# Optimization experiments

Hardware: AMD Instinct MI355X
Metric: run time of the kernel (lower is better)

## Reference

```python
import jax, jax.numpy as jnp
import numpy as np

NX, NY = 512, 1024  # scaled grid (source used 128x256)
HID = 32


def _grid_edges(nx, ny):
    """Bidirectional 4-neighbor grid adjacency as [2, E] int32."""
    idx = np.arange(nx * ny).reshape(nx, ny)
    h_s, h_t = idx[:, :-1].ravel(), idx[:, 1:].ravel()
    v_s, v_t = idx[:-1, :].ravel(), idx[1:, :].ravel()
    src = np.concatenate([h_s, h_t, v_s, v_t])
    dst = np.concatenate([h_t, h_s, v_t, v_s])
    return jnp.asarray(np.stack([src, dst]), dtype=jnp.int32)


def setup_inputs() -> dict:
    key = jax.random.key(0)
    ks = jax.random.split(key, 8)

    def lin(k, fan_in, fan_out):
        bound = 1.0 / np.sqrt(fan_in)
        kw, kb = jax.random.split(k)
        w = jax.random.uniform(kw, (fan_in, fan_out), jnp.float32, -bound, bound)
        b = jax.random.uniform(kb, (fan_out,), jnp.float32, -bound, bound)
        return w, b

    inp = {}
    inp["x"] = jax.random.normal(ks[0], (NX * NY, 4), jnp.float32)
    inp["edge_index_0"] = _grid_edges(NX, NY)
    inp["edge_index_1"] = _grid_edges(NX // 2, NY // 2)
    inp["edge_index_2"] = _grid_edges(NX // 4, NY // 4)
    inp["fc1_w"], inp["fc1_b"] = lin(ks[1], 4, HID)
    for i in range(1, 6):
        inp[f"w{i}"], inp[f"b{i}"] = lin(ks[1 + i], HID, HID)
    inp["fc2_w"], inp["fc2_b"] = lin(ks[7], HID, 2)
    return inp


def gcn_conv(x, edge_index, w, b):
    """PyG GCNConv: self-loops + symmetric norm + linear + scatter-add + bias."""
    n = x.shape[0]
    loop = jnp.arange(n, dtype=edge_index.dtype)
    src = jnp.concatenate([edge_index[0], loop])
    dst = jnp.concatenate([edge_index[1], loop])
    deg = jax.ops.segment_sum(jnp.ones(dst.shape, x.dtype), dst, num_segments=n)
    dis = jax.lax.rsqrt(deg)  # deg >= 1 because of self-loops
    norm = dis[src] * dis[dst]  # [E+N]
    xw = x @ w  # [N, HID]
    out = jax.ops.segment_sum(xw[src] * norm[:, None], dst, num_segments=n)
    return out + b


def _upsample2(x):
    # Buffer-exact replica of torch `upsample(x, dim=2, channels=32, scale=2)`:
    # with `channels` doubling between iterations; then transpose + reshape.
    x = x.T  # [32, N]
    ch = HID
    for _ in range(2):
        x = jnp.repeat(x.reshape(ch, -1), 2, axis=-1)
        ch *= 2
    return x.T.reshape(-1, HID)  # [4N, 32]


def reference(x, edge_index_0, edge_index_1, edge_index_2,
              fc1_w, fc1_b, w1, b1, w2, b2, w3, b3, w4, b4, w5, b5,
              fc2_w, fc2_b):
    nx1, ny1 = NX // 2, NY // 2
    h = jax.nn.relu(x @ fc1_w + fc1_b)
    h = jax.nn.relu(gcn_conv(h, edge_index_0, w1, b1))            # level 0
    h1 = h.reshape(NX, NY, HID)[::2, ::2, :].reshape(-1, HID)     # down to level 1
    h1 = jax.nn.relu(gcn_conv(h1, edge_index_1, w2, b2))
    h2 = h1.reshape(nx1, ny1, HID)[::2, ::2, :].reshape(-1, HID)  # down to level 2
    h2 = jax.nn.relu(gcn_conv(h2, edge_index_2, w3, b3))
    h1u = h1 + _upsample2(h2)                                     # up to level 1
    h1u = jax.nn.relu(gcn_conv(h1u, edge_index_1, w4, b4))
    hu = h + _upsample2(h1u)                                      # up to level 0
    hu = jax.nn.relu(gcn_conv(hu, edge_index_0, w5, b5))
    return hu @ fc2_w + fc2_b  # [NX*NY, 2]
```

## Files before the change

### kernel.cpp

```cpp
#include <hip/hip_runtime.h>


#define TI 4
#define TJ 32

typedef float v2f __attribute__((ext_vector_type(2)));

__device__ __forceinline__ v2f pka(v2f a, v2f b) {
  v2f d; asm("v_pk_add_f32 %0, %1, %2" : "=v"(d) : "v"(a), "v"(b)); return d;
}
__device__ __forceinline__ v2f pkm(v2f a, v2f b) {
  v2f d; asm("v_pk_mul_f32 %0, %1, %2" : "=v"(d) : "v"(a), "v"(b)); return d;
}
__device__ __forceinline__ v2f relu2(v2f a) {
  v2f d; d.x = fmaxf(a.x, 0.f); d.y = fmaxf(a.y, 0.f); return d;
}
__device__ __forceinline__ v2f pkfma_bl(v2f a, v2f b, v2f c) {
  v2f d;
  asm("v_pk_fma_f32 %0, %1, %2, %3 op_sel:[0,0,0] op_sel_hi:[0,1,1]"
      : "=v"(d) : "v"(a), "v"(b), "v"(c));
  return d;
}
__device__ __forceinline__ v2f pkfma_bh(v2f a, v2f b, v2f c) {
  v2f d;
  asm("v_pk_fma_f32 %0, %1, %2, %3 op_sel:[1,0,0] op_sel_hi:[1,1,1]"
      : "=v"(d) : "v"(a), "v"(b), "v"(c));
  return d;
}

__device__ __forceinline__ v2f LOq(const float4& f) { return *(const v2f*)&f.x; }
__device__ __forceinline__ v2f HIq(const float4& f) { return *(const v2f*)&f.z; }
__device__ __forceinline__ float4 MK4(v2f lo, v2f hi) {
  return make_float4(lo.x, lo.y, hi.x, hi.y);
}
__device__ __forceinline__ float4 p4add(float4 a, float4 b) {
  return MK4(pka(LOq(a), LOq(b)), pka(HIq(a), HIq(b)));
}

__device__ __forceinline__ float disf(int i, int j, int nx, int ny) {
  int deg = 1 + (i > 0) + (i < nx - 1) + (j > 0) + (j < ny - 1);
  return rsqrtf((float)deg);
}
__device__ __forceinline__ float4 f4z() { return make_float4(0.f, 0.f, 0.f, 0.f); }

template <int MODE, int NX, int NY, int NLOW>
__device__ __forceinline__ float4 load_u(
    const float* __restrict__ src, const float* __restrict__ low,
    const float4 (&f1c)[4], const float4& f1b, int gi, int gj, int c) {
  if (gi < 0 || gi >= NX || gj < 0 || gj >= NY) return f4z();
  const float d = disf(gi, gj, NX, NY);
  if constexpr (MODE == 0) {
    const float4 xv = ((const float4*)src)[gi * NY + gj];
    const v2f x01 = LOq(xv), x23 = HIq(xv);
    v2f h01 = LOq(f1b), h23 = HIq(f1b);
    h01 = pkfma_bl(x01, LOq(f1c[0]), h01); h23 = pkfma_bl(x01, HIq(f1c[0]), h23);
    h01 = pkfma_bh(x01, LOq(f1c[1]), h01); h23 = pkfma_bh(x01, HIq(f1c[1]), h23);
    h01 = pkfma_bl(x23, LOq(f1c[2]), h01); h23 = pkfma_bl(x23, HIq(f1c[2]), h23);
    h01 = pkfma_bh(x23, LOq(f1c[3]), h01); h23 = pkfma_bh(x23, HIq(f1c[3]), h23);
    h01 = relu2(h01); h23 = relu2(h23);
    v2f dp; dp.x = d; dp.y = d;
    return MK4(pkm(dp, h01), pkm(dp, h23));
  } else if constexpr (MODE == 1) {
    const float4 v = ((const float4*)src)[((size_t)(2 * gi) * (2 * NY) + 2 * gj) * 8 + c];
    v2f dp; dp.x = d; dp.y = d;
    return MK4(pkm(dp, LOq(v)), pkm(dp, HIq(v)));
  } else {
    const int r = gi * NY + gj;
    float4 v = ((const float4*)src)[(size_t)r * 8 + c];
    const int col = 16 * (r & 1) + 2 * c;
    const float2 E = *(const float2*)(low + (size_t)(r >> 3) * 32 + col);
    const float2 O = *(const float2*)(low + (size_t)((NLOW + (r >> 2)) >> 1) * 32 + col);
    v.x = (v.x + E.x) * d; v.y = (v.y + O.x) * d;
    v.z = (v.z + E.y) * d; v.w = (v.w + O.y) * d;
    return v;
  }
}

template <int MODE, int NX, int NY, int NLOW>
__global__ __launch_bounds__(256, 6) void fused_gcn(
    const float* __restrict__ src, const float* __restrict__ low,
    const float* __restrict__ w, const float* __restrict__ bias,
    const float* __restrict__ fc1w, const float* __restrict__ fc1b,
    const float* __restrict__ fw2, const float* __restrict__ fb2,
    float* __restrict__ out) {
  __shared__ __align__(16) float sT[32][TI * TJ + 2];
  __shared__ __align__(16) float ldsW[1024];
  __shared__ __align__(16) float ldsB[104];

  const int t = threadIdx.x;
  ((float4*)ldsW)[t] = ((const float4*)w)[t];
  if (t < 32) ldsB[t] = bias[t];
  if constexpr (MODE == 3) {
    if (t >= 32 && t < 96) ldsB[t] = fw2[t - 32];
    if (t >= 96 && t < 98) ldsB[t] = fb2[t - 96];
  }

  constexpr int GX = NY / TJ;
  constexpr int GY = NX / TI;
  constexpr int NWG = GX * GY;
  constexpr int LGX = (GX == 8) ? 3 : ((GX == 16) ? 4 : 5);
  const int bid = blockIdx.y * GX + blockIdx.x;
  const int sw = (bid & 7) * (NWG >> 3) + (bid >> 3);
  const int j0 = (sw & (GX - 1)) * TJ;
  const int i0 = (sw >> LGX) * TI;

  const int jn = t >> 3, c = t & 7;
  const int gj = j0 + jn;

  float4 f1c[4], f1b;
  if constexpr (MODE == 0) {
#pragma unroll
    for (int r = 0; r < 4; ++r) f1c[r] = *(const float4*)(fc1w + r * 32 + 4 * c);
    f1b = *(const float4*)(fc1b + 4 * c);
  }
  auto LOADU = [&](int a, int b) -> float4 {
    return load_u<MODE, NX, NY, NLOW>(src, low, f1c, f1b, a, b, c);
  };

  float4 up = LOADU(i0 - 1, gj);
  float4 uc = LOADU(i0, gj);
  float4 un = LOADU(i0 + 1, gj);
  float4 lf = LOADU(i0, gj - 1);
  float4 rt = LOADU(i0, gj + 1);

#pragma unroll
  for (int i = 0; i < TI; ++i) {
    const float4 sv = p4add(p4add(p4add(up, uc), p4add(un, lf)), rt);
    const int n = i * TJ + jn;
    sT[4 * c + 0][n] = sv.x; sT[4 * c + 1][n] = sv.y;
    sT[4 * c + 2][n] = sv.z; sT[4 * c + 3][n] = sv.w;
    if (i < TI - 1) {
      up = uc; uc = un;
      un = LOADU(i0 + i + 2, gj);
      lf = LOADU(i0 + i + 1, gj - 1);
      rt = LOADU(i0 + i + 1, gj + 1);
    }
  }
  __syncthreads();

  const int p = t >> 2, tc = t & 3;
  v2f oA[4] = {{0.f, 0.f}, {0.f, 0.f}, {0.f, 0.f}, {0.f, 0.f}};
  v2f oB[4] = {{0.f, 0.f}, {0.f, 0.f}, {0.f, 0.f}, {0.f, 0.f}};
#pragma unroll
  for (int k = 0; k < 32; ++k) {
    const v2f sp = *(const v2f*)&sT[k][2 * p];
    const float4 w0 = *(const float4*)&ldsW[k * 32 + 8 * tc];
    const float4 w1 = *(const float4*)&ldsW[k * 32 + 8 * tc + 4];
    const v2f w00 = LOq(w0), w01 = HIq(w0), w10 = LOq(w1), w11 = HIq(w1);
    oA[0] = pkfma_bl(sp, w00, oA[0]); oA[1] = pkfma_bl(sp, w01, oA[1]);
    oA[2] = pkfma_bl(sp, w10, oA[2]); oA[3] = pkfma_bl(sp, w11, oA[3]);
    oB[0] = pkfma_bh(sp, w00, oB[0]); oB[1] = pkfma_bh(sp, w01, oB[1]);
    oB[2] = pkfma_bh(sp, w10, oB[2]); oB[3] = pkfma_bh(sp, w11, oB[3]);
  }

  const int nA = 2 * p;
  const int gi = i0 + (nA >> 5);
  const int gjA = j0 + (nA & 31);
  const float dA = disf(gi, gjA, NX, NY);
  const float dB = disf(gi, gjA + 1, NX, NY);
  v2f dAp; dAp.x = dA; dAp.y = dA;
  v2f dBp; dBp.x = dB; dBp.y = dB;

  v2f bp[4];
  bp[0] = *(const v2f*)&ldsB[8 * tc];     bp[1] = *(const v2f*)&ldsB[8 * tc + 2];
  bp[2] = *(const v2f*)&ldsB[8 * tc + 4]; bp[3] = *(const v2f*)&ldsB[8 * tc + 6];

  v2f vA[4], vB[4];
#pragma unroll
  for (int q = 0; q < 4; ++q) {
    vA[q] = relu2(pkfma_bl(dAp, oA[q], bp[q]));
    vB[q] = relu2(pkfma_bl(dBp, oB[q], bp[q]));
  }

  if constexpr (MODE != 3) {
    float* opA = out + (size_t)(gi * NY + gjA) * 32 + 8 * tc;
    *(float4*)opA = MK4(vA[0], vA[1]);
    *(float4*)(opA + 4) = MK4(vA[2], vA[3]);
    *(float4*)(opA + 32) = MK4(vB[0], vB[1]);
    *(float4*)(opA + 36) = MK4(vB[2], vB[3]);
  } else {
    v2f accA = {0.f, 0.f}, accB = {0.f, 0.f};
#pragma unroll
    for (int q = 0; q < 4; ++q) {
      const v2f f0 = *(const v2f*)&ldsB[32 + 16 * tc + 4 * q];
      const v2f f1 = *(const v2f*)&ldsB[32 + 16 * tc + 4 * q + 2];
      accA = pkfma_bl(vA[q], f0, accA); accA = pkfma_bh(vA[q], f1, accA);
      accB = pkfma_bl(vB[q], f0, accB); accB = pkfma_bh(vB[q], f1, accB);
    }
#pragma unroll
    for (int m = 1; m <= 2; m <<= 1) {
      accA.x += __shfl_xor(accA.x, m, 64); accA.y += __shfl_xor(accA.y, m, 64);
      accB.x += __shfl_xor(accB.x, m, 64); accB.y += __shfl_xor(accB.y, m, 64);
    }
    if (tc == 0) {
      const v2f fb = *(const v2f*)&ldsB[96];
      accA = pka(accA, fb); accB = pka(accB, fb);
      ((float4*)out)[(gi * NY + gjA) >> 1] = MK4(accA, accB);
    }
  }
}

#define N0 (512 * 1024)
#define N1 (256 * 512)
#define N2 (128 * 256)

extern "C" void kernel_launch(void* const* d_in, const int* in_sizes, int n_in,
                              void* d_out, int out_size, void* d_ws, size_t ws_size,
                              hipStream_t stream) {
  const float* x    = (const float*)d_in[0];
  const float* fc1w = (const float*)d_in[4];
  const float* fc1b = (const float*)d_in[5];
  const float* w1 = (const float*)d_in[6];
  const float* b1 = (const float*)d_in[7];
  const float* w2 = (const float*)d_in[8];
  const float* b2 = (const float*)d_in[9];
  const float* w3 = (const float*)d_in[10];
  const float* b3 = (const float*)d_in[11];
  const float* w4 = (const float*)d_in[12];
  const float* b4 = (const float*)d_in[13];
  const float* w5 = (const float*)d_in[14];
  const float* b5 = (const float*)d_in[15];
  const float* fw2 = (const float*)d_in[16];
  const float* fb2 = (const float*)d_in[17];

  float* ws = (float*)d_ws;
  const size_t S0 = (size_t)N0 * 32, S1 = (size_t)N1 * 32, S2 = (size_t)N2 * 32;
  float* h   = ws;
  float* h1  = ws + S0;
  float* h2  = ws + S0 + S1;
  float* h1u = ws + S0 + S1 + S2;
  float* outp = (float*)d_out;

  fused_gcn<0, 512, 1024, 0><<<dim3(1024 / TJ, 512 / TI), 256, 0, stream>>>(
      x, nullptr, w1, b1, fc1w, fc1b, nullptr, nullptr, h);
  fused_gcn<1, 256, 512, 0><<<dim3(512 / TJ, 256 / TI), 256, 0, stream>>>(
      h, nullptr, w2, b2, nullptr, nullptr, nullptr, nullptr, h1);
  fused_gcn<1, 128, 256, 0><<<dim3(256 / TJ, 128 / TI), 256, 0, stream>>>(
      h1, nullptr, w3, b3, nullptr, nullptr, nullptr, nullptr, h2);
  fused_gcn<2, 256, 512, N2><<<dim3(512 / TJ, 256 / TI), 256, 0, stream>>>(
      h1, h2, w4, b4, nullptr, nullptr, nullptr, nullptr, h1u);
  fused_gcn<3, 512, 1024, N1><<<dim3(1024 / TJ, 512 / TI), 256, 0, stream>>>(
      h, h1u, w5, b5, nullptr, nullptr, fw2, fb2, outp);
}
```

Measured before the change: 198.9 us.

## Double row tile and compute four nodes per thread in GCN matmul

Raises the tile height from 4 to 8 rows so each thread computes 4 nodes × 8 outputs, loading a float4 of aggregated features per k-step instead of a float2. The goal is more FMAs per LDS weight load and more rows of vertical stencil reuse per tile, with fewer halo reloads. The shared-memory channel layout is permuted and its stride padded to limit bank conflicts. In exchange it uses more registers and LDS per block, so launch bounds drop from 6 to 4 waves per SIMD, which lowers occupancy.

```diff
diff --git a/kernel.cpp b/kernel.cpp
--- a/kernel.cpp
+++ b/kernel.cpp
@@ -1,8 +1,9 @@
 #include <hip/hip_runtime.h>
 
 
-#define TI 4
+#define TI 8
 #define TJ 32
+#define SSTR (TI * TJ + 4)
 
 typedef float v2f __attribute__((ext_vector_type(2)));
 
@@ -77,13 +78,13 @@
 }
 
 template <int MODE, int NX, int NY, int NLOW>
-__global__ __launch_bounds__(256, 6) void fused_gcn(
+__global__ __launch_bounds__(256, 4) void fused_gcn(
     const float* __restrict__ src, const float* __restrict__ low,
     const float* __restrict__ w, const float* __restrict__ bias,
     const float* __restrict__ fc1w, const float* __restrict__ fc1b,
     const float* __restrict__ fw2, const float* __restrict__ fb2,
     float* __restrict__ out) {
-  __shared__ __align__(16) float sT[32][TI * TJ + 2];
+  __shared__ __align__(16) float sT[32][SSTR];
   __shared__ __align__(16) float ldsW[1024];
   __shared__ __align__(16) float ldsB[104];
 
@@ -127,8 +128,10 @@
   for (int i = 0; i < TI; ++i) {
     const float4 sv = p4add(p4add(p4add(up, uc), p4add(un, lf)), rt);
     const int n = i * TJ + jn;
-    sT[4 * c + 0][n] = sv.x; sT[4 * c + 1][n] = sv.y;
-    sT[4 * c + 2][n] = sv.z; sT[4 * c + 3][n] = sv.w;
+    sT[c][n]      = sv.x;
+    sT[c + 8][n]  = sv.y;
+    sT[c + 16][n] = sv.z;
+    sT[c + 24][n] = sv.w;
     if (i < TI - 1) {
       up = uc; uc = un;
       un = LOADU(i0 + i + 2, gj);
@@ -138,64 +141,81 @@
   }
   __syncthreads();
 
-  const int p = t >> 2, tc = t & 3;
-  v2f oA[4] = {{0.f, 0.f}, {0.f, 0.f}, {0.f, 0.f}, {0.f, 0.f}};
-  v2f oB[4] = {{0.f, 0.f}, {0.f, 0.f}, {0.f, 0.f}, {0.f, 0.f}};
+  const int q = t >> 2, tc = t & 3;
+  v2f o[4][4];
+#pragma unroll
+  for (int m = 0; m < 4; ++m)
+#pragma unroll
+    for (int j = 0; j < 4; ++j) { o[m][j].x = 0.f; o[m][j].y = 0.f; }
+
 #pragma unroll
   for (int k = 0; k < 32; ++k) {
-    const v2f sp = *(const v2f*)&sT[k][2 * p];
+    const int r = (k >> 2) + 8 * (k & 3);
+    const float4 sp = *(const float4*)&sT[r][4 * q];
     const float4 w0 = *(const float4*)&ldsW[k * 32 + 8 * tc];
     const float4 w1 = *(const float4*)&ldsW[k * 32 + 8 * tc + 4];
+    const v2f sp01 = LOq(sp), sp23 = HIq(sp);
     const v2f w00 = LOq(w0), w01 = HIq(w0), w10 = LOq(w1), w11 = HIq(w1);
-    oA[0] = pkfma_bl(sp, w00, oA[0]); oA[1] = pkfma_bl(sp, w01, oA[1]);
-    oA[2] = pkfma_bl(sp, w10, oA[2]); oA[3] = pkfma_bl(sp, w11, oA[3]);
-    oB[0] = pkfma_bh(sp, w00, oB[0]); oB[1] = pkfma_bh(sp, w01, oB[1]);
-    oB[2] = pkfma_bh(sp, w10, oB[2]); oB[3] = pkfma_bh(sp, w11, oB[3]);
-  }
-
-  const int nA = 2 * p;
-  const int gi = i0 + (nA >> 5);
-  const int gjA = j0 + (nA & 31);
-  const float dA = disf(gi, gjA, NX, NY);
-  const float dB = disf(gi, gjA + 1, NX, NY);
-  v2f dAp; dAp.x = dA; dAp.y = dA;
-  v2f dBp; dBp.x = dB; dBp.y = dB;
+    o[0][0] = pkfma_bl(sp01, w00, o[0][0]); o[0][1] = pkfma_bl(sp01, w01, o[0][1]);
+    o[0][2] = pkfma_bl(sp01, w10, o[0][2]); o[0][3] = pkfma_bl(sp01, w11, o[0][3]);
+    o[1][0] = pkfma_bh(sp01, w00, o[1][0]); o[1][1] = pkfma_bh(sp01, w01, o[1][1]);
+    o[1][2] = pkfma_bh(sp01, w10, o[1][2]); o[1][3] = pkfma_bh(sp01, w11, o[1][3]);
+    o[2][0] = pkfma_bl(sp23, w00, o[2][0]); o[2][1] = pkfma_bl(sp23, w01, o[2][1]);
+    o[2][2] = pkfma_bl(sp23, w10, o[2][2]); o[2][3] = pkfma_bl(sp23, w11, o[2][3]);
+    o[3][0] = pkfma_bh(sp23, w00, o[3][0]); o[3][1] = pkfma_bh(sp23, w01, o[3][1]);
+    o[3][2] = pkfma_bh(sp23, w10, o[3][2]); o[3][3] = pkfma_bh(sp23, w11, o[3][3]);
+  }
+
+  const int nb = 4 * q;
+  const int gi = i0 + (nb >> 5);
+  const int gj0 = j0 + (nb & 31);
 
   v2f bp[4];
   bp[0] = *(const v2f*)&ldsB[8 * tc];     bp[1] = *(const v2f*)&ldsB[8 * tc + 2];
   bp[2] = *(const v2f*)&ldsB[8 * tc + 4]; bp[3] = *(const v2f*)&ldsB[8 * tc + 6];
 
-  v2f vA[4], vB[4];
-#pragma unroll
-  for (int q = 0; q < 4; ++q) {
-    vA[q] = relu2(pkfma_bl(dAp, oA[q], bp[q]));
-    vB[q] = relu2(pkfma_bl(dBp, oB[q], bp[q]));
+  v2f vv[4][4];
+#pragma unroll
+  for (int m = 0; m < 4; ++m) {
+    const float dm = disf(gi, gj0 + m, NX, NY);
+    v2f dp; dp.x = dm; dp.y = dm;
+#pragma unroll
+    for (int j = 0; j < 4; ++j) vv[m][j] = relu2(pkfma_bl(dp, o[m][j], bp[j]));
   }
 
   if constexpr (MODE != 3) {
-    float* opA = out + (size_t)(gi * NY + gjA) * 32 + 8 * tc;
-    *(float4*)opA = MK4(vA[0], vA[1]);
-    *(float4*)(opA + 4) = MK4(vA[2], vA[3]);
-    *(float4*)(opA + 32) = MK4(vB[0], vB[1]);
-    *(float4*)(opA + 36) = MK4(vB[2], vB[3]);
+#pragma unroll
+    for (int m = 0; m < 4; ++m) {
+      float* op = out + (size_t)(gi * NY + gj0 + m) * 32 + 8 * tc;
+      *(float4*)op = MK4(vv[m][0], vv[m][1]);
+      *(float4*)(op + 4) = MK4(vv[m][2], vv[m][3]);
+    }
   } else {
-    v2f accA = {0.f, 0.f}, accB = {0.f, 0.f};
-#pragma unroll
-    for (int q = 0; q < 4; ++q) {
-      const v2f f0 = *(const v2f*)&ldsB[32 + 16 * tc + 4 * q];
-      const v2f f1 = *(const v2f*)&ldsB[32 + 16 * tc + 4 * q + 2];
-      accA = pkfma_bl(vA[q], f0, accA); accA = pkfma_bh(vA[q], f1, accA);
-      accB = pkfma_bl(vB[q], f0, accB); accB = pkfma_bh(vB[q], f1, accB);
-    }
-#pragma unroll
-    for (int m = 1; m <= 2; m <<= 1) {
-      accA.x += __shfl_xor(accA.x, m, 64); accA.y += __shfl_xor(accA.y, m, 64);
-      accB.x += __shfl_xor(accB.x, m, 64); accB.y += __shfl_xor(accB.y, m, 64);
+    v2f fw[4][2];
+#pragma unroll
+    for (int j = 0; j < 4; ++j) {
+      fw[j][0] = *(const v2f*)&ldsB[32 + 16 * tc + 4 * j];
+      fw[j][1] = *(const v2f*)&ldsB[32 + 16 * tc + 4 * j + 2];
+    }
+    v2f acc[4];
+#pragma unroll
+    for (int m = 0; m < 4; ++m) {
+      acc[m].x = 0.f; acc[m].y = 0.f;
+#pragma unroll
+      for (int j = 0; j < 4; ++j) {
+        acc[m] = pkfma_bl(vv[m][j], fw[j][0], acc[m]);
+        acc[m] = pkfma_bh(vv[m][j], fw[j][1], acc[m]);
+      }
+      acc[m].x += __shfl_xor(acc[m].x, 1, 64); acc[m].x += __shfl_xor(acc[m].x, 2, 64);
+      acc[m].y += __shfl_xor(acc[m].y, 1, 64); acc[m].y += __shfl_xor(acc[m].y, 2, 64);
     }
     if (tc == 0) {
       const v2f fb = *(const v2f*)&ldsB[96];
-      accA = pka(accA, fb); accB = pka(accB, fb);
-      ((float4*)out)[(gi * NY + gjA) >> 1] = MK4(accA, accB);
+#pragma unroll
+      for (int m = 0; m < 4; ++m) acc[m] = pka(acc[m], fb);
+      float4* ob = (float4*)out + ((gi * NY + gj0) >> 1);
+      ob[0] = MK4(acc[0], acc[1]);
+      ob[1] = MK4(acc[2], acc[3]);
     }
   }
 }
```

New measurement: 218.4 us. 9.8% more time.
